# Performance work log

Measured on AMD Instinct MI355X. Metric: run time of the kernel, lower is better.

## Reference

```python
import jax, jax.numpy as jnp
import numpy as np

N_NODES = 50000
N_EDGES = 800000
IN_SIZE = 128
HID = 128
OUT_SIZE = 64
N_LAYERS = 2
MAXK = 32


def setup_inputs() -> dict:
    key = jax.random.key(0)
    ks = jax.random.split(key, 8)
    s = 0.05  # small init scale, xavier-like
    return {
        "x": jax.random.normal(ks[0], (N_NODES, IN_SIZE), dtype=jnp.float32),
        "W_in": jax.random.normal(ks[1], (IN_SIZE, HID), dtype=jnp.float32) * s,
        "b_in": jnp.zeros((HID,), dtype=jnp.float32),
        "W_self": jax.random.normal(ks[2], (N_LAYERS, HID, HID), dtype=jnp.float32) * s,
        "W_neigh": jax.random.normal(ks[3], (N_LAYERS, HID, HID), dtype=jnp.float32) * s,
        "W_out": jax.random.normal(ks[4], (HID, OUT_SIZE), dtype=jnp.float32) * s,
        "b_out": jnp.zeros((OUT_SIZE,), dtype=jnp.float32),
        "edge_index": jax.random.randint(ks[5], (2, N_EDGES), 0, N_NODES, dtype=jnp.int32),
        "k": MAXK,
    }


def _maxk(x, k):
    # Keep top-k values per row, zero out the rest (MaxK nonlinearity).
    vals, idx = jax.lax.top_k(x, k)                     # [N, k]
    rows = jnp.arange(x.shape[0])[:, None]
    return jnp.zeros_like(x).at[rows, idx].set(vals)


def reference(x, W_in, b_in, W_self, W_neigh, W_out, b_out, edge_index, k):
    N = x.shape[0]
    src, dst = edge_index[0], edge_index[1]
    # Row sums of the (src->dst) adjacency = out-degree of src, per original code.
    deg = jax.ops.segment_sum(jnp.ones((src.shape[0],), dtype=x.dtype), src,
                              num_segments=N)[:, None]  # [N, 1]
    h = x @ W_in + b_in                                  # lin_in
    for i in range(W_self.shape[0]):
        hs = _maxk(h, k)                                 # MaxK sparsify [N, H]
        # adj @ hs : out[i] = sum over edges (i -> j) of hs[j]; then mean-normalize
        agg = jax.ops.segment_sum(hs[dst], src, num_segments=N) / (deg + 1e-6)
        h = hs @ W_self[i] + agg @ W_neigh[i]            # h_self + h_neigh
        # dropout (eval) and Identity norm are no-ops
    return h @ W_out + b_out                             # lin_out
```

## Files before the change

### kernel.cpp

```cpp
#include <hip/hip_runtime.h>

#define KDIM 128

typedef _Float16 f16x8 __attribute__((ext_vector_type(8)));
typedef _Float16 f16x4 __attribute__((ext_vector_type(4)));
typedef float f32x16 __attribute__((ext_vector_type(16)));

__global__ void hist_kernel(const int* __restrict__ src, int* __restrict__ cnt, int E) {
    int i = blockIdx.x * blockDim.x + threadIdx.x;
    if (i < E) atomicAdd(&cnt[src[i]], 1);
}

__global__ void scan_kernel(const int* __restrict__ cnt, int* __restrict__ row_ptr,
                            int* __restrict__ cursor, int N) {
    __shared__ int wsum[16];
    __shared__ int base_sh;
    const int tid = threadIdx.x;
    const int lane = tid & 63;
    const int w = tid >> 6;
    if (tid == 0) base_sh = 0;
    __syncthreads();
    for (int base = 0; base < N; base += 1024) {
        int i = base + tid;
        int v = (i < N) ? cnt[i] : 0;
        int x = v;
        #pragma unroll
        for (int off = 1; off < 64; off <<= 1) {
            int t = __shfl_up(x, off);
            if (lane >= off) x += t;
        }
        if (lane == 63) wsum[w] = x;
        __syncthreads();
        if (tid < 16) {
            int t = wsum[tid];
            #pragma unroll
            for (int off = 1; off < 16; off <<= 1) {
                int u = __shfl_up(t, off);
                if (tid >= off) t += u;
            }
            wsum[tid] = t;
        }
        __syncthreads();
        int wexcl = (w == 0) ? 0 : wsum[w - 1];
        int excl = base_sh + wexcl + (x - v);
        if (i < N) { row_ptr[i] = excl; cursor[i] = excl; }
        int total = wsum[15];
        __syncthreads();
        if (tid == 0) base_sh += total;
        __syncthreads();
    }
    if (threadIdx.x == 0) row_ptr[N] = base_sh;
}

__global__ void scatter_kernel(const int* __restrict__ src, const int* __restrict__ dst,
                               int* cursor, int* __restrict__ col, int E) {
    int i = blockIdx.x * blockDim.x + threadIdx.x;
    if (i < E) {
        int p = atomicAdd(&cursor[src[i]], 1);
        col[p] = dst[i];
    }
}

__global__ void sortrows_kernel(const int* __restrict__ row_ptr, int* __restrict__ col, int M) {
    int wid = (blockIdx.x * blockDim.x + threadIdx.x) >> 6;
    int lane = threadIdx.x & 63;
    if (wid >= M) return;
    int s = row_ptr[wid], e = row_ptr[wid + 1], len = e - s;
    if (len <= 1) return;
    if (len <= 64) {
        int v = (lane < len) ? col[s + lane] : 0x7fffffff;
        #pragma unroll
        for (int k = 2; k <= 64; k <<= 1) {
            #pragma unroll
            for (int j = k >> 1; j > 0; j >>= 1) {
                int o = __shfl_xor(v, j);
                bool dir = ((lane & k) == 0);
                bool smaller = ((lane & j) == 0);
                int mn = min(v, o), mx = max(v, o);
                v = (dir == smaller) ? mn : mx;
            }
        }
        if (lane < len) col[s + lane] = v;
    } else if (lane == 0) {
        for (int a = s + 1; a < e; a++) {
            int key = col[a];
            int b = a - 1;
            while (b >= s && col[b] > key) { col[b + 1] = col[b]; b--; }
            col[b + 1] = key;
        }
    }
}

__global__ void maxk_kernel(const float* __restrict__ h, float* __restrict__ hs, int M) {
    int wid = (blockIdx.x * blockDim.x + threadIdx.x) >> 6;
    int lane = threadIdx.x & 63;
    if (wid >= M) return;
    float2 v = ((const float2*)(h + (size_t)wid * KDIM))[lane];

    unsigned int u0 = __float_as_uint(v.x);
    u0 = (u0 & 0x80000000u) ? ~u0 : (u0 | 0x80000000u);
    unsigned int u1 = __float_as_uint(v.y);
    u1 = (u1 & 0x80000000u) ? ~u1 : (u1 | 0x80000000u);

    unsigned int prefix = 0;
    int remaining = 32;
    #pragma unroll
    for (int b = 31; b >= 0; --b) {
        unsigned int candHi = (prefix >> b) | 1u;
        unsigned long long m0 = __ballot((u0 >> b) == candHi);
        unsigned long long m1 = __ballot((u1 >> b) == candHi);
        int cnt = __popcll(m0) + __popcll(m1);
        if (cnt >= remaining) prefix |= (1u << b);
        else remaining -= cnt;
    }

    unsigned long long e0 = __ballot(u0 == prefix);
    unsigned long long e1 = __ballot(u1 == prefix);
    unsigned long long g0 = __ballot(u0 > prefix);
    unsigned long long g1 = __ballot(u1 > prefix);
    int quota = 32 - (__popcll(g0) + __popcll(g1));
    unsigned long long below = (1ULL << lane) - 1ULL;
    int rank0 = __popcll(e0 & below) + __popcll(e1 & below);
    int rank1 = rank0 + (int)((e0 >> lane) & 1ULL);
    bool k0 = (u0 > prefix) || (((e0 >> lane) & 1ULL) && rank0 < quota);
    bool k1 = (u1 > prefix) || (((e1 >> lane) & 1ULL) && rank1 < quota);

    float2 o;
    o.x = k0 ? v.x : 0.0f;
    o.y = k1 ? v.y : 0.0f;
    ((float2*)(hs + (size_t)wid * KDIM))[lane] = o;
}

__global__ __launch_bounds__(256)
void aggregate_kernel(const float* __restrict__ hs, const int* __restrict__ row_ptr,
                      const int* __restrict__ col, float* __restrict__ agg, int M) {
    const int lane = threadIdx.x & 63;
    const int wid = (blockIdx.x * blockDim.x + threadIdx.x) >> 6;
    if (wid >= M) return;
    const int half = lane >> 5;
    const int l32 = lane & 31;
    const int s = row_ptr[wid], e = row_ptr[wid + 1];
    const float4* __restrict__ hp = (const float4*)hs;

    float4 a0 = make_float4(0.f, 0.f, 0.f, 0.f);
    float4 a1 = a0, a2 = a0, a3 = a0;

    int j = s + half;
    for (; j + 6 < e; j += 8) {
        int c0 = col[j];
        int c1 = col[j + 2];
        int c2 = col[j + 4];
        int c3 = col[j + 6];
        float4 v0 = hp[(size_t)c0 * 32 + l32];
        float4 v1 = hp[(size_t)c1 * 32 + l32];
        float4 v2 = hp[(size_t)c2 * 32 + l32];
        float4 v3 = hp[(size_t)c3 * 32 + l32];
        a0.x += v0.x; a0.y += v0.y; a0.z += v0.z; a0.w += v0.w;
        a1.x += v1.x; a1.y += v1.y; a1.z += v1.z; a1.w += v1.w;
        a2.x += v2.x; a2.y += v2.y; a2.z += v2.z; a2.w += v2.w;
        a3.x += v3.x; a3.y += v3.y; a3.z += v3.z; a3.w += v3.w;
    }
    for (; j < e; j += 2) {
        int c = col[j];
        float4 v = hp[(size_t)c * 32 + l32];
        a0.x += v.x; a0.y += v.y; a0.z += v.z; a0.w += v.w;
    }

    float4 t;
    t.x = ((a0.x + a1.x) + a2.x) + a3.x;
    t.y = ((a0.y + a1.y) + a2.y) + a3.y;
    t.z = ((a0.z + a1.z) + a2.z) + a3.z;
    t.w = ((a0.w + a1.w) + a2.w) + a3.w;

    float4 u;
    u.x = __shfl_xor(t.x, 32);
    u.y = __shfl_xor(t.y, 32);
    u.z = __shfl_xor(t.z, 32);
    u.w = __shfl_xor(t.w, 32);

    if (half == 0) {
        float inv = 1.0f / ((float)(e - s) + 1e-6f);
        float4 o;
        o.x = (t.x + u.x) * inv;
        o.y = (t.y + u.y) * inv;
        o.z = (t.z + u.z) * inv;
        o.w = (t.w + u.w) * inv;
        ((float4*)(agg + (size_t)wid * KDIM))[l32] = o;
    }
}

__global__ void conv_wt_kernel(const float* __restrict__ W_in,
                               const float* __restrict__ W_self,
                               const float* __restrict__ W_neigh,
                               const float* __restrict__ W_out,
                               _Float16* __restrict__ wb) {
    int t = blockIdx.x * blockDim.x + threadIdx.x;
    if (t < 81920) {
        int m = t >> 14;
        int e = t & 16383;
        int n = e >> 7, k = e & 127;
        const float* S = (m == 0) ? W_in
                       : (m <= 2) ? (W_self + (size_t)(m - 1) * 16384)
                                  : (W_neigh + (size_t)(m - 3) * 16384);
        float v = S[k * 128 + n];
        _Float16 hi = (_Float16)v;
        _Float16 lo = (_Float16)(v - (float)hi);
        int pair = m * 2;
        wb[(size_t)pair * 16384 + n * 128 + k] = hi;
        wb[(size_t)(pair + 1) * 16384 + n * 128 + k] = lo;
    } else if (t < 90112) {
        int e = t - 81920;
        int n = e >> 7, k = e & 127;
        float v = W_out[k * 64 + n];
        _Float16 hi = (_Float16)v;
        _Float16 lo = (_Float16)(v - (float)hi);
        wb[(size_t)10 * 16384 + e] = hi;
        wb[(size_t)11 * 16384 + e] = lo;
    }
}

template <int BN, bool DUAL, bool BIAS>
__global__ __launch_bounds__(256)
void gemm_mfma(const float* __restrict__ A1, const float* __restrict__ A2,
               const _Float16* __restrict__ B1h, const _Float16* __restrict__ B1l,
               const _Float16* __restrict__ B2h, const _Float16* __restrict__ B2l,
               const float* __restrict__ bias, float* __restrict__ C, int M) {
    constexpr int NSRC = DUAL ? 2 : 1;
    constexpr int NT = BN / 32;
    constexpr int TPW = NT / 2;

    __shared__ __align__(16) char Alds[NSRC * 2 * 64 * 256];

    const int tid = threadIdx.x;
    const int w = tid >> 6;
    const int lane = tid & 63;
    const int l31 = lane & 31;
    const int kslot = lane >> 5;
    const int row0 = blockIdx.x * 64;

    for (int s = 0; s < NSRC; s++) {
        const float* A = s ? A2 : A1;
        #pragma unroll
        for (int p = 0; p < 8; p++) {
            int idx = tid + p * 256;
            int row = idx >> 5, k4 = idx & 31;
            float4 v = make_float4(0.f, 0.f, 0.f, 0.f);
            if (row0 + row < M) v = *(const float4*)(A + (size_t)(row0 + row) * KDIM + k4 * 4);
            _Float16 h0 = (_Float16)v.x, h1 = (_Float16)v.y,
                     h2 = (_Float16)v.z, h3 = (_Float16)v.w;
            f16x4 hv = {h0, h1, h2, h3};
            f16x4 lv = {(_Float16)(v.x - (float)h0), (_Float16)(v.y - (float)h1),
                        (_Float16)(v.z - (float)h2), (_Float16)(v.w - (float)h3)};
            int boff = (k4 * 8) ^ ((row & 7) << 4);
            *(f16x4*)(Alds + (s * 2 + 0) * 16384 + row * 256 + boff) = hv;
            *(f16x4*)(Alds + (s * 2 + 1) * 16384 + row * 256 + boff) = lv;
        }
    }
    __syncthreads();

    const int n0 = (BN == 128) ? w * 32 : (w & 1) * 32;
    const int mt0 = (BN == 128) ? 0 : (w >> 1);

    f32x16 acc[TPW];
    #pragma unroll
    for (int t = 0; t < TPW; t++)
        #pragma unroll
        for (int e = 0; e < 16; e++) acc[t][e] = 0.0f;

    for (int s = 0; s < NSRC; s++) {
        const _Float16* Bh = s ? B2h : B1h;
        const _Float16* Bl = s ? B2l : B1l;
        const _Float16* bph = Bh + (size_t)(n0 + l31) * 128 + kslot * 8;
        const _Float16* bpl = Bl + (size_t)(n0 + l31) * 128 + kslot * 8;
        const char* abase = Alds + (size_t)(s * 2) * 16384;
        #pragma unroll
        for (int kb = 0; kb < 8; kb++) {
            f16x8 bh = *(const f16x8*)(bph + kb * 16);
            f16x8 bl = *(const f16x8*)(bpl + kb * 16);
            #pragma unroll
            for (int t = 0; t < TPW; t++) {
                int row = (mt0 + t) * 32 + l31;
                int boff = ((kb * 2 + kslot) * 16) ^ ((row & 7) << 4);
                const char* rp = abase + row * 256 + boff;
                f16x8 ah = *(const f16x8*)(rp);
                f16x8 al = *(const f16x8*)(rp + 16384);
                acc[t] = __builtin_amdgcn_mfma_f32_32x32x16_f16(al, bh, acc[t], 0, 0, 0);
                acc[t] = __builtin_amdgcn_mfma_f32_32x32x16_f16(ah, bl, acc[t], 0, 0, 0);
                acc[t] = __builtin_amdgcn_mfma_f32_32x32x16_f16(ah, bh, acc[t], 0, 0, 0);
            }
        }
    }

    float bv = 0.0f;
    if (BIAS) bv = bias[n0 + l31];
    #pragma unroll
    for (int t = 0; t < TPW; t++) {
        #pragma unroll
        for (int r = 0; r < 16; r++) {
            int row = row0 + (mt0 + t) * 32 + (r & 3) + 8 * (r >> 2) + 4 * kslot;
            if (row < M) C[(size_t)row * BN + n0 + l31] = acc[t][r] + bv;
        }
    }
}

extern "C" void kernel_launch(void* const* d_in, const int* in_sizes, int n_in,
                              void* d_out, int out_size, void* d_ws, size_t ws_size,
                              hipStream_t stream) {
    const float* x       = (const float*)d_in[0];
    const float* W_in    = (const float*)d_in[1];
    const float* b_in    = (const float*)d_in[2];
    const float* W_self  = (const float*)d_in[3];
    const float* W_neigh = (const float*)d_in[4];
    const float* W_out   = (const float*)d_in[5];
    const float* b_out   = (const float*)d_in[6];
    const int*   eidx    = (const int*)d_in[7];

    const int N = 50000, E = 800000;
    const int* src = eidx;
    const int* dst = eidx + E;

    char* ws = (char*)d_ws;
    float* h   = (float*)(ws);
    float* hs  = (float*)(ws + 25600000);
    float* agg = (float*)(ws + 51200000);
    int* cnt     = (int*)(ws + 76800000);
    int* row_ptr = (int*)(ws + 77000000);
    int* cursor  = (int*)(ws + 77200016);
    int* col     = (int*)(ws + 77400016);
    _Float16* wb = (_Float16*)(ws + 80600016);

    const _Float16* WinT_h  = wb + (size_t)0 * 16384;
    const _Float16* WinT_l  = wb + (size_t)1 * 16384;
    const _Float16* WoutT_h = wb + (size_t)10 * 16384;
    const _Float16* WoutT_l = wb + (size_t)11 * 16384;

    hipMemsetAsync(cnt, 0, N * sizeof(int), stream);
    hist_kernel<<<(E + 255) / 256, 256, 0, stream>>>(src, cnt, E);
    scan_kernel<<<1, 1024, 0, stream>>>(cnt, row_ptr, cursor, N);
    scatter_kernel<<<(E + 255) / 256, 256, 0, stream>>>(src, dst, cursor, col, E);
    sortrows_kernel<<<(N + 3) / 4, 256, 0, stream>>>(row_ptr, col, N);
    conv_wt_kernel<<<(90112 + 255) / 256, 256, 0, stream>>>(W_in, W_self, W_neigh, W_out, wb);

    const int G = (N + 63) / 64;

    gemm_mfma<128, false, true><<<G, 256, 0, stream>>>(
        x, nullptr, WinT_h, WinT_l, nullptr, nullptr, b_in, h, N);

    for (int i = 0; i < 2; i++) {
        maxk_kernel<<<(N + 3) / 4, 256, 0, stream>>>(h, hs, N);
        aggregate_kernel<<<(N + 3) / 4, 256, 0, stream>>>(hs, row_ptr, col, agg, N);
        const _Float16* WsT_h = wb + (size_t)(2 + 2 * i) * 16384;
        const _Float16* WsT_l = wb + (size_t)(3 + 2 * i) * 16384;
        const _Float16* WnT_h = wb + (size_t)(6 + 2 * i) * 16384;
        const _Float16* WnT_l = wb + (size_t)(7 + 2 * i) * 16384;
        gemm_mfma<128, true, false><<<G, 256, 0, stream>>>(
            hs, agg, WsT_h, WsT_l, WnT_h, WnT_l, nullptr, h, N);
    }

    gemm_mfma<64, false, true><<<G, 256, 0, stream>>>(
        h, nullptr, WoutT_h, WoutT_l, nullptr, nullptr, b_out, (float*)d_out, N);
}
```

Baseline: 431.6 us.

## Parallelize CSR row-pointer scan and partition histogram/scatter atomics by node range

```diff
diff --git a/kernel.cpp b/kernel.cpp
--- a/kernel.cpp
+++ b/kernel.cpp
@@ -6,59 +6,87 @@
 typedef _Float16 f16x4 __attribute__((ext_vector_type(4)));
 typedef float f32x16 __attribute__((ext_vector_type(16)));
 
+#define NRANGE 6250
+#define ECHUNK 3200
+
 __global__ void hist_kernel(const int* __restrict__ src, int* __restrict__ cnt, int E) {
-    int i = blockIdx.x * blockDim.x + threadIdx.x;
-    if (i < E) atomicAdd(&cnt[src[i]], 1);
-}
-
-__global__ void scan_kernel(const int* __restrict__ cnt, int* __restrict__ row_ptr,
-                            int* __restrict__ cursor, int N) {
-    __shared__ int wsum[16];
-    __shared__ int base_sh;
-    const int tid = threadIdx.x;
-    const int lane = tid & 63;
-    const int w = tid >> 6;
-    if (tid == 0) base_sh = 0;
-    __syncthreads();
-    for (int base = 0; base < N; base += 1024) {
-        int i = base + tid;
-        int v = (i < N) ? cnt[i] : 0;
-        int x = v;
-        #pragma unroll
-        for (int off = 1; off < 64; off <<= 1) {
-            int t = __shfl_up(x, off);
-            if (lane >= off) x += t;
-        }
-        if (lane == 63) wsum[w] = x;
-        __syncthreads();
-        if (tid < 16) {
-            int t = wsum[tid];
-            #pragma unroll
-            for (int off = 1; off < 16; off <<= 1) {
-                int u = __shfl_up(t, off);
-                if (tid >= off) t += u;
-            }
-            wsum[tid] = t;
-        }
-        __syncthreads();
-        int wexcl = (w == 0) ? 0 : wsum[w - 1];
-        int excl = base_sh + wexcl + (x - v);
-        if (i < N) { row_ptr[i] = excl; cursor[i] = excl; }
-        int total = wsum[15];
-        __syncthreads();
-        if (tid == 0) base_sh += total;
-        __syncthreads();
-    }
-    if (threadIdx.x == 0) row_ptr[N] = base_sh;
+    const int r = blockIdx.x & 7;
+    const int chunk = blockIdx.x >> 3;
+    const int lo = r * NRANGE, hi = lo + NRANGE;
+    const int base = chunk * ECHUNK;
+    const int end = min(base + ECHUNK, E);
+    for (int i = base + threadIdx.x; i < end; i += 256) {
+        int s = src[i];
+        if (s >= lo && s < hi) atomicAdd(&cnt[s], 1);
+    }
 }
 
 __global__ void scatter_kernel(const int* __restrict__ src, const int* __restrict__ dst,
                                int* cursor, int* __restrict__ col, int E) {
-    int i = blockIdx.x * blockDim.x + threadIdx.x;
-    if (i < E) {
-        int p = atomicAdd(&cursor[src[i]], 1);
-        col[p] = dst[i];
-    }
+    const int r = blockIdx.x & 7;
+    const int chunk = blockIdx.x >> 3;
+    const int lo = r * NRANGE, hi = lo + NRANGE;
+    const int base = chunk * ECHUNK;
+    const int end = min(base + ECHUNK, E);
+    for (int i = base + threadIdx.x; i < end; i += 256) {
+        int s = src[i];
+        if (s >= lo && s < hi) {
+            int p = atomicAdd(&cursor[s], 1);
+            col[p] = dst[i];
+        }
+    }
+}
+
+__global__ void scan1_kernel(const int* __restrict__ cnt, int* __restrict__ row_ptr,
+                             int* __restrict__ bsum, int N) {
+    __shared__ int ws[4];
+    const int t = threadIdx.x;
+    const int lane = t & 63, w = t >> 6;
+    const int i = blockIdx.x * 256 + t;
+    int v = (i < N) ? cnt[i] : 0;
+    int x = v;
+    #pragma unroll
+    for (int off = 1; off < 64; off <<= 1) {
+        int u = __shfl_up(x, off);
+        if (lane >= off) x += u;
+    }
+    if (lane == 63) ws[w] = x;
+    __syncthreads();
+    int wexcl = 0;
+    #pragma unroll
+    for (int k = 0; k < 4; k++) wexcl += (k < w) ? ws[k] : 0;
+    if (i < N) row_ptr[i] = wexcl + x - v;
+    if (t == 255) bsum[blockIdx.x] = wexcl + x;
+}
+
+__global__ void scan2_kernel(int* __restrict__ bsum, int NB) {
+    __shared__ int ws[4];
+    const int t = threadIdx.x;
+    const int lane = t & 63, w = t >> 6;
+    int v = (t < NB) ? bsum[t] : 0;
+    int x = v;
+    #pragma unroll
+    for (int off = 1; off < 64; off <<= 1) {
+        int u = __shfl_up(x, off);
+        if (lane >= off) x += u;
+    }
+    if (lane == 63) ws[w] = x;
+    __syncthreads();
+    int wexcl = 0;
+    #pragma unroll
+    for (int k = 0; k < 4; k++) wexcl += (k < w) ? ws[k] : 0;
+    if (t < NB) bsum[t] = wexcl + x - v;
+}
+
+__global__ void scan3_kernel(const int* __restrict__ bsum, int* __restrict__ row_ptr,
+                             int* __restrict__ cursor, int N, int E) {
+    const int i = blockIdx.x * 256 + threadIdx.x;
+    if (i < N) {
+        int v = row_ptr[i] + bsum[blockIdx.x];
+        row_ptr[i] = v;
+        cursor[i] = v;
+    }
+    if (i == 0) row_ptr[N] = E;
 }
 
 __global__ void sortrows_kernel(const int* __restrict__ row_ptr, int* __restrict__ col, int M) {
@@ -328,16 +356,22 @@
     int* cursor  = (int*)(ws + 77200016);
     int* col     = (int*)(ws + 77400016);
     _Float16* wb = (_Float16*)(ws + 80600016);
+    int* bsum    = (int*)(ws + 81000016);
 
     const _Float16* WinT_h  = wb + (size_t)0 * 16384;
     const _Float16* WinT_l  = wb + (size_t)1 * 16384;
     const _Float16* WoutT_h = wb + (size_t)10 * 16384;
     const _Float16* WoutT_l = wb + (size_t)11 * 16384;
 
+    const int NB = (N + 255) / 256;
+    const int EG = ((E + ECHUNK - 1) / ECHUNK) * 8;
+
     hipMemsetAsync(cnt, 0, N * sizeof(int), stream);
-    hist_kernel<<<(E + 255) / 256, 256, 0, stream>>>(src, cnt, E);
-    scan_kernel<<<1, 1024, 0, stream>>>(cnt, row_ptr, cursor, N);
-    scatter_kernel<<<(E + 255) / 256, 256, 0, stream>>>(src, dst, cursor, col, E);
+    hist_kernel<<<EG, 256, 0, stream>>>(src, cnt, E);
+    scan1_kernel<<<NB, 256, 0, stream>>>(cnt, row_ptr, bsum, N);
+    scan2_kernel<<<1, 256, 0, stream>>>(bsum, NB);
+    scan3_kernel<<<NB, 256, 0, stream>>>(bsum, row_ptr, cursor, N, E);
+    scatter_kernel<<<EG, 256, 0, stream>>>(src, dst, cursor, col, E);
     sortrows_kernel<<<(N + 3) / 4, 256, 0, stream>>>(row_ptr, col, N);
     conv_wt_kernel<<<(90112 + 255) / 256, 256, 0, stream>>>(W_in, W_self, W_neigh, W_out, wb);
 
```

After: 375.9 us. -12.9%, faster.
